# Kernel tuning notes

Hardware: AMD Instinct MI355X
Metric: run time of the kernel (lower is better)

## Reference

```python
import jax, jax.numpy as jnp
import numpy as np

BN_EPS = 1e-5

def _bn(h, g, b):
    # BatchNorm1d training-mode math: biased batch stats over the node axis.
    m = h.mean(axis=0)
    v = h.var(axis=0)
    return (h - m) * jax.lax.rsqrt(v + BN_EPS) * g + b

def setup_inputs() -> dict:
    key = jax.random.key(0)
    ks = jax.random.split(key, 8)
    N, E, D_IN, H, L = 50000, 800000, 128, 256, 3
    return {
        "x": jax.random.normal(ks[0], (N, D_IN), dtype=jnp.float32),
        "edge_index": jax.random.randint(ks[1], (2, E), 0, N, dtype=jnp.int64),
        "eps": jnp.zeros((L,), dtype=jnp.float32),
        "W1_0": jax.random.normal(ks[2], (D_IN, H), dtype=jnp.float32),
        "W1_rest": jax.random.normal(ks[3], (L - 1, H, H), dtype=jnp.float32),
        "b1": jnp.zeros((L, H), dtype=jnp.float32),
        "g1": jnp.ones((L, H), dtype=jnp.float32),
        "bt1": jnp.zeros((L, H), dtype=jnp.float32),
        "W2": jax.random.normal(ks[4], (L, H, H), dtype=jnp.float32),
        "b2": jnp.zeros((L, H), dtype=jnp.float32),
        "g2": jnp.ones((L, H), dtype=jnp.float32),
        "bt2": jnp.zeros((L, H), dtype=jnp.float32),
    }

def reference(x, edge_index, eps, W1_0, W1_rest, b1, g1, bt1, W2, b2, g2, bt2):
    N = x.shape[0]
    row, col = edge_index[0], edge_index[1]
    L = eps.shape[0]

    def gin_layer(h, eps_i, Wa, ba, ga, bta, Wb, bb, gb, btb):
        # sum_{u in N(v)} h_u : gather source feats, scatter-add to dest rows
        agg = jax.ops.segment_sum(h[col], row, num_segments=N)
        out = (1.0 + eps_i) * h + agg
        out = _bn(out @ Wa + ba, ga, bta)        # Linear -> BN
        out = jax.nn.relu(out)                    # ReLU
        out = _bn(out @ Wb + bb, gb, btb)        # Linear -> BN
        return out

    h = x
    for i in range(L):
        Wa = W1_0 if i == 0 else W1_rest[i - 1]
        h = gin_layer(h, eps[i], Wa, b1[i], g1[i], bt1[i], W2[i], b2[i], g2[i], bt2[i])
        if i < L - 1:
            h = jax.nn.relu(h)  # inter-layer ReLU; dropout is identity in eval mode
    return h
```

## Files before the change

### kernel.cpp

```cpp
#include <hip/hip_runtime.h>
#include <hip/hip_bf16.h>
#include <math.h>
#include <stdint.h>

typedef short short8 __attribute__((ext_vector_type(8)));
typedef float f32x4 __attribute__((ext_vector_type(4)));

__device__ __forceinline__ float bf2f(unsigned int u) {
    union { unsigned int i; float f; } x; x.i = u << 16; return x.f;
}
__device__ __forceinline__ unsigned short f2bf(float f) {
    union { float f; unsigned int i; } x; x.f = f;
    unsigned int r = x.i + 0x7fffu + ((x.i >> 16) & 1u);
    return (unsigned short)(r >> 16);
}

__global__ void hist_k(const int* __restrict__ row, int* __restrict__ deg, int E) {
    int e = blockIdx.x * blockDim.x + threadIdx.x;
    if (e < E) atomicAdd(&deg[row[e]], 1);
}
__global__ void block_sums(const int* __restrict__ deg, int* __restrict__ bs, int N) {
    __shared__ int tmp[256];
    int t = threadIdx.x;
    int i = blockIdx.x * 256 + t;
    tmp[t] = (i < N) ? deg[i] : 0;
    __syncthreads();
    for (int off = 128; off > 0; off >>= 1) {
        if (t < off) tmp[t] += tmp[t + off];
        __syncthreads();
    }
    if (t == 0) bs[blockIdx.x] = tmp[0];
}
__global__ void scan_bs(const int* __restrict__ bs, int* __restrict__ bo, int B) {
    __shared__ int tmp[256];
    int t = threadIdx.x;
    int v = (t < B) ? bs[t] : 0;
    tmp[t] = v;
    __syncthreads();
    for (int off = 1; off < 256; off <<= 1) {
        int x = (t >= off) ? tmp[t - off] : 0;
        __syncthreads();
        tmp[t] += x;
        __syncthreads();
    }
    bo[t] = tmp[t] - v;
}
__global__ void finalize_rowptr(const int* __restrict__ deg, const int* __restrict__ bo,
                                int* __restrict__ rowptr, int* __restrict__ cursor,
                                int N, int E) {
    __shared__ int tmp[256];
    int t = threadIdx.x;
    int i = blockIdx.x * 256 + t;
    int v = (i < N) ? deg[i] : 0;
    tmp[t] = v;
    __syncthreads();
    for (int off = 1; off < 256; off <<= 1) {
        int x = (t >= off) ? tmp[t - off] : 0;
        __syncthreads();
        tmp[t] += x;
        __syncthreads();
    }
    int excl = tmp[t] - v + bo[blockIdx.x];
    if (i < N) { rowptr[i] = excl; cursor[i] = excl; }
    if (i == N) rowptr[N] = E;
}
__global__ void fill_csr(const int* __restrict__ row, const int* __restrict__ col,
                         int* __restrict__ cursor, int* __restrict__ idx, int E) {
    int e = blockIdx.x * blockDim.x + threadIdx.x;
    if (e < E) {
        int p = atomicAdd(&cursor[row[e]], 1);
        idx[p] = col[e];
    }
}

__global__ void zero_all(int* __restrict__ deg, int n_deg,
                         uint4* __restrict__ a, uint4* __restrict__ b, uint4* __restrict__ c,
                         int n_t, uint4* __restrict__ st, int n_st) {
    int i = blockIdx.x * blockDim.x + threadIdx.x;
    uint4 z = make_uint4(0, 0, 0, 0);
    if (i < n_deg) deg[i] = 0;
    if (i < n_t) { a[i] = z; b[i] = z; c[i] = z; }
    if (i < n_st) st[i] = z;
}

__global__ void prep_all(const float* __restrict__ x, unsigned short* __restrict__ xb, int nconv,
                         const float* __restrict__ W1_0, const float* __restrict__ W1rest,
                         const float* __restrict__ W2, unsigned short* __restrict__ wt) {
    int i = blockIdx.x * blockDim.x + threadIdx.x;
    if (i < nconv) {
        float4 v = *(const float4*)(x + (size_t)i * 4);
        unsigned int lo = (unsigned int)f2bf(v.x) | ((unsigned int)f2bf(v.y) << 16);
        unsigned int hi = (unsigned int)f2bf(v.z) | ((unsigned int)f2bf(v.w) << 16);
        *(uint2*)(xb + (size_t)i * 4) = make_uint2(lo, hi);
        return;
    }
    int id = i - nconv;
    if (id < 32768) {
        int k = id >> 8, c = id & 255;
        wt[c * 128 + k] = f2bf(W1_0[id]);
    } else if (id < 163840) {
        int t = id - 32768;
        int m = t >> 16, r = t & 65535;
        int k = r >> 8, c = r & 255;
        wt[32768 + m * 65536 + c * 256 + k] = f2bf(W1rest[t]);
    } else if (id < 360448) {
        int t = id - 163840;
        int m = t >> 16, r = t & 65535;
        int k = r >> 8, c = r & 255;
        wt[163840 + m * 65536 + c * 256 + k] = f2bf(W2[t]);
    }
}

template<int H, bool FUSE_BN>
__global__ __launch_bounds__(256) void aggregate_f(
    const unsigned short* __restrict__ h,
    const int* __restrict__ rowptr, const int* __restrict__ idx,
    const float* __restrict__ eps_p, int layer,
    const float* __restrict__ stats, const float* __restrict__ g,
    const float* __restrict__ bt, float invN,
    unsigned short* __restrict__ out, int N) {
    constexpr int NW = H / 128;
    int lane = threadIdx.x & 63;
    int v = blockIdx.x * 4 + (threadIdx.x >> 6);
    if (v >= N) return;

    float sc[2 * NW], sh[2 * NW];
    if constexpr (FUSE_BN) {
#pragma unroll
        for (int j = 0; j < 2 * NW; ++j) {
            int c = lane * 2 * NW + j;
            float m = stats[c] * invN;
            float var = stats[256 + c] * invN - m * m;
            sc[j] = g[c] * rsqrtf(var + 1e-5f);
            sh[j] = bt[c] - m * sc[j];
        }
    }
    const float s = 1.f + eps_p[layer];
    const unsigned int* hu = (const unsigned int*)h;

    float acc[2 * NW];
    {
        const unsigned int* hv = hu + (size_t)v * (H / 2) + lane * NW;
#pragma unroll
        for (int j = 0; j < NW; ++j) {
            unsigned int r = hv[j];
            float f0 = bf2f(r & 0xffffu), f1 = bf2f(r >> 16);
            if constexpr (FUSE_BN) {
                f0 = fmaxf(f0 * sc[2 * j] + sh[2 * j], 0.f);
                f1 = fmaxf(f1 * sc[2 * j + 1] + sh[2 * j + 1], 0.f);
            }
            acc[2 * j] = s * f0;
            acc[2 * j + 1] = s * f1;
        }
    }
    int e = rowptr[v], end = rowptr[v + 1];
    for (; e + 3 < end; e += 4) {
        int u0 = idx[e], u1 = idx[e + 1], u2 = idx[e + 2], u3 = idx[e + 3];
        const unsigned int* q0 = hu + (size_t)u0 * (H / 2) + lane * NW;
        const unsigned int* q1 = hu + (size_t)u1 * (H / 2) + lane * NW;
        const unsigned int* q2 = hu + (size_t)u2 * (H / 2) + lane * NW;
        const unsigned int* q3 = hu + (size_t)u3 * (H / 2) + lane * NW;
        unsigned int r0[NW], r1[NW], r2[NW], r3[NW];
#pragma unroll
        for (int j = 0; j < NW; ++j) { r0[j] = q0[j]; r1[j] = q1[j]; r2[j] = q2[j]; r3[j] = q3[j]; }
#pragma unroll
        for (int j = 0; j < NW; ++j) {
            float a0 = bf2f(r0[j] & 0xffffu), b0 = bf2f(r0[j] >> 16);
            float a1 = bf2f(r1[j] & 0xffffu), b1 = bf2f(r1[j] >> 16);
            float a2 = bf2f(r2[j] & 0xffffu), b2 = bf2f(r2[j] >> 16);
            float a3 = bf2f(r3[j] & 0xffffu), b3 = bf2f(r3[j] >> 16);
            if constexpr (FUSE_BN) {
                float c0 = sc[2 * j], d0 = sh[2 * j], c1 = sc[2 * j + 1], d1 = sh[2 * j + 1];
                a0 = fmaxf(a0 * c0 + d0, 0.f); b0 = fmaxf(b0 * c1 + d1, 0.f);
                a1 = fmaxf(a1 * c0 + d0, 0.f); b1 = fmaxf(b1 * c1 + d1, 0.f);
                a2 = fmaxf(a2 * c0 + d0, 0.f); b2 = fmaxf(b2 * c1 + d1, 0.f);
                a3 = fmaxf(a3 * c0 + d0, 0.f); b3 = fmaxf(b3 * c1 + d1, 0.f);
            }
            acc[2 * j]     += (a0 + a1) + (a2 + a3);
            acc[2 * j + 1] += (b0 + b1) + (b2 + b3);
        }
    }
    for (; e < end; ++e) {
        const unsigned int* q = hu + (size_t)idx[e] * (H / 2) + lane * NW;
#pragma unroll
        for (int j = 0; j < NW; ++j) {
            unsigned int r = q[j];
            float f0 = bf2f(r & 0xffffu), f1 = bf2f(r >> 16);
            if constexpr (FUSE_BN) {
                f0 = fmaxf(f0 * sc[2 * j] + sh[2 * j], 0.f);
                f1 = fmaxf(f1 * sc[2 * j + 1] + sh[2 * j + 1], 0.f);
            }
            acc[2 * j] += f0;
            acc[2 * j + 1] += f1;
        }
    }
    unsigned int* op = (unsigned int*)out + (size_t)v * (H / 2) + lane * NW;
#pragma unroll
    for (int j = 0; j < NW; ++j)
        op[j] = (unsigned int)f2bf(acc[2 * j]) | ((unsigned int)f2bf(acc[2 * j + 1]) << 16);
}

template<int K, bool TRANS_A>
__global__ __launch_bounds__(256) void gemm_mfma(const unsigned short* __restrict__ A,
                                                 const unsigned short* __restrict__ Wt,
                                                 const float* __restrict__ bias,
                                                 const float* __restrict__ stats_in,
                                                 const float* __restrict__ gp,
                                                 const float* __restrict__ btp,
                                                 float invN,
                                                 unsigned short* __restrict__ Y,
                                                 float* __restrict__ stats_out,
                                                 int Nrows) {
    __shared__ unsigned short sA[2][128 * 32];
    __shared__ unsigned short sB[2][128 * 32];
    __shared__ float reds[128], redq[128];
    __shared__ float spc[256], sps[256];
    const int tid = threadIdx.x;
    const int lane = tid & 63;
    const int wid = tid >> 6;
    const int wm = wid >> 1, wn = wid & 1;
    const int r0 = blockIdx.x * 128;
    const int c0 = blockIdx.y * 128;
    const int chunk0 = wid * 2;
    const int akk = (lane & 3) * 8;
    const int arow_l = lane >> 2;

    if constexpr (TRANS_A) {
        float m = stats_in[tid] * invN;
        float var = stats_in[256 + tid] * invN - m * m;
        float sv = gp[tid] * rsqrtf(var + 1e-5f);
        spc[tid] = sv;
        sps[tid] = btp[tid] - m * sv;
        __syncthreads();
    }

    f32x4 acc[4][4] = {};

    auto stageB = [&](int buf, int k0) {
#pragma unroll
        for (int q = 0; q < 2; ++q) {
            int chunk = chunk0 + q;
            int byteoff = chunk * 1024 + lane * 16;
            int row = byteoff >> 6;
            int kk = (byteoff & 63) >> 1;
            const unsigned short* gB = Wt + (size_t)(c0 + row) * K + k0 + kk;
            __builtin_amdgcn_global_load_lds(
                (const __attribute__((address_space(1))) void*)(uintptr_t)gB,
                (__attribute__((address_space(3))) void*)(uintptr_t)(&sB[buf][chunk * 512]),
                16, 0, 0);
        }
    };
    auto stageA_direct = [&](int buf, int k0) {
#pragma unroll
        for (int q = 0; q < 2; ++q) {
            int chunk = chunk0 + q;
            int byteoff = chunk * 1024 + lane * 16;
            int row = byteoff >> 6;
            int kk = (byteoff & 63) >> 1;
            const unsigned short* gA = A + (size_t)(r0 + row) * K + k0 + kk;
            __builtin_amdgcn_global_load_lds(
                (const __attribute__((address_space(1))) void*)(uintptr_t)gA,
                (__attribute__((address_space(3))) void*)(uintptr_t)(&sA[buf][chunk * 512]),
                16, 0, 0);
        }
    };
    uint4 areg[2];
    auto loadA = [&](int k0) {
#pragma unroll
        for (int q = 0; q < 2; ++q) {
            int row = (chunk0 + q) * 16 + arow_l;
            areg[q] = *(const uint4*)(A + (size_t)(r0 + row) * K + k0 + akk);
        }
    };
    auto writeA = [&](int buf, int k0) {
        float4 sca = *(const float4*)&spc[k0 + akk];
        float4 scb = *(const float4*)&spc[k0 + akk + 4];
        float4 sha = *(const float4*)&sps[k0 + akk];
        float4 shb = *(const float4*)&sps[k0 + akk + 4];
#pragma unroll
        for (int q = 0; q < 2; ++q) {
            uint4 u = areg[q];
            float f0 = fmaxf(bf2f(u.x & 0xffffu) * sca.x + sha.x, 0.f);
            float f1 = fmaxf(bf2f(u.x >> 16)     * sca.y + sha.y, 0.f);
            float f2 = fmaxf(bf2f(u.y & 0xffffu) * sca.z + sha.z, 0.f);
            float f3 = fmaxf(bf2f(u.y >> 16)     * sca.w + sha.w, 0.f);
            float f4 = fmaxf(bf2f(u.z & 0xffffu) * scb.x + shb.x, 0.f);
            float f5 = fmaxf(bf2f(u.z >> 16)     * scb.y + shb.y, 0.f);
            float f6 = fmaxf(bf2f(u.w & 0xffffu) * scb.z + shb.z, 0.f);
            float f7 = fmaxf(bf2f(u.w >> 16)     * scb.w + shb.w, 0.f);
            uint4 w;
            w.x = (unsigned int)f2bf(f0) | ((unsigned int)f2bf(f1) << 16);
            w.y = (unsigned int)f2bf(f2) | ((unsigned int)f2bf(f3) << 16);
            w.z = (unsigned int)f2bf(f4) | ((unsigned int)f2bf(f5) << 16);
            w.w = (unsigned int)f2bf(f6) | ((unsigned int)f2bf(f7) << 16);
            *(uint4*)&sA[buf][(chunk0 + q) * 512 + lane * 8] = w;
        }
    };

    const int nt = K / 32;
    if constexpr (TRANS_A) { loadA(0); } else { stageA_direct(0, 0); }
    stageB(0, 0);
    const int krow = lane >> 4;
    const int rl = lane & 15;

    for (int t = 0; t < nt; ++t) {
        if constexpr (TRANS_A) writeA(t & 1, t * 32);
        __syncthreads();
        if (t + 1 < nt) {
            stageB((t + 1) & 1, (t + 1) * 32);
            if constexpr (TRANS_A) loadA((t + 1) * 32);
            else stageA_direct((t + 1) & 1, (t + 1) * 32);
        }
        const unsigned short* sAb = sA[t & 1];
        const unsigned short* sBb = sB[t & 1];
        short8 a[4], b[4];
#pragma unroll
        for (int i = 0; i < 4; ++i) {
            a[i] = *(const short8*)(sAb + (wm * 64 + i * 16 + rl) * 32 + krow * 8);
            b[i] = *(const short8*)(sBb + (wn * 64 + i * 16 + rl) * 32 + krow * 8);
        }
#pragma unroll
        for (int i = 0; i < 4; ++i)
#pragma unroll
            for (int n = 0; n < 4; ++n)
                asm volatile("v_mfma_f32_16x16x32_bf16 %0, %1, %2, %0"
                             : "+v"(acc[i][n])
                             : "v"(a[i]), "v"(b[n]));
    }
    asm volatile("s_nop 7\n\ts_nop 7" ::);

    const int rg = lane >> 4;
    float ssum[4], qsum[4];
#pragma unroll
    for (int n = 0; n < 4; ++n) {
        int col = c0 + wn * 64 + n * 16 + rl;
        float bvv = bias[col];
        float s = 0.f, q2 = 0.f;
#pragma unroll
        for (int i = 0; i < 4; ++i) {
#pragma unroll
            for (int r = 0; r < 4; ++r) {
                int grow = r0 + wm * 64 + i * 16 + rg * 4 + r;
                if (grow < Nrows) {
                    float v = acc[i][n][r] + bvv;
                    Y[(size_t)grow * 256 + col] = f2bf(v);
                    s += v;
                    q2 += v * v;
                }
            }
        }
        s  += __shfl_xor(s, 16, 64);  s  += __shfl_xor(s, 32, 64);
        q2 += __shfl_xor(q2, 16, 64); q2 += __shfl_xor(q2, 32, 64);
        ssum[n] = s; qsum[n] = q2;
    }
    if (wm == 0 && rg == 0) {
#pragma unroll
        for (int n = 0; n < 4; ++n) {
            int lc = wn * 64 + n * 16 + rl;
            reds[lc] = ssum[n];
            redq[lc] = qsum[n];
        }
    }
    __syncthreads();
    if (wm == 1 && rg == 0) {
#pragma unroll
        for (int n = 0; n < 4; ++n) {
            int lc = wn * 64 + n * 16 + rl;
            int c = c0 + lc;
            atomicAdd(&stats_out[c], ssum[n] + reds[lc]);
            atomicAdd(&stats_out[256 + c], qsum[n] + redq[lc]);
        }
    }
}

__global__ void bn_fuse(const unsigned short* __restrict__ Y, const float* __restrict__ stats,
                        const float* __restrict__ g, const float* __restrict__ bt,
                        float invN, float* __restrict__ outf, int total8) {
    int i = blockIdx.x * blockDim.x + threadIdx.x;
    if (i >= total8) return;
    int col0 = (i & 31) << 3;
    uint4 y = ((const uint4*)Y)[i];
    unsigned int yy[4] = {y.x, y.y, y.z, y.w};
    float o[8];
#pragma unroll
    for (int j = 0; j < 4; ++j) {
        o[2 * j]     = bf2f(yy[j] & 0xffffu);
        o[2 * j + 1] = bf2f(yy[j] >> 16);
    }
#pragma unroll
    for (int j = 0; j < 8; ++j) {
        int c = col0 + j;
        float mean = stats[c] * invN;
        float var = stats[256 + c] * invN - mean * mean;
        float sc = g[c] * rsqrtf(var + 1e-5f);
        float sh = bt[c] - mean * sc;
        o[j] = o[j] * sc + sh;
    }
    float4* of = (float4*)outf;
    of[2 * i]     = make_float4(o[0], o[1], o[2], o[3]);
    of[2 * i + 1] = make_float4(o[4], o[5], o[6], o[7]);
}

extern "C" void kernel_launch(void* const* d_in, const int* in_sizes, int n_in,
                              void* d_out, int out_size, void* d_ws, size_t ws_size,
                              hipStream_t stream) {
    const float* x      = (const float*)d_in[0];
    const int*   ei     = (const int*)d_in[1];
    const float* eps    = (const float*)d_in[2];
    const float* W1_0   = (const float*)d_in[3];
    const float* W1rest = (const float*)d_in[4];
    const float* b1     = (const float*)d_in[5];
    const float* g1     = (const float*)d_in[6];
    const float* bt1    = (const float*)d_in[7];
    const float* W2     = (const float*)d_in[8];
    const float* b2     = (const float*)d_in[9];
    const float* g2     = (const float*)d_in[10];
    const float* bt2    = (const float*)d_in[11];

    const int N = in_sizes[0] / 128;
    const int E = in_sizes[1] / 2;
    const int* row = ei;
    const int* col = ei + E;
    const int Npad = ((N + 127) / 128) * 128;
    const int nbRow = Npad / 128;

    char* w = (char*)d_ws;
    auto alloc = [&](size_t bytes) {
        char* p = w;
        w += (bytes + 255) & ~(size_t)255;
        return p;
    };
    unsigned short* xb = (unsigned short*)alloc((size_t)Npad * 128 * 2);
    unsigned short* p0 = (unsigned short*)alloc((size_t)Npad * 256 * 2);
    unsigned short* p1 = (unsigned short*)alloc((size_t)Npad * 256 * 2);
    unsigned short* Yb = (unsigned short*)alloc((size_t)Npad * 256 * 2);
    unsigned short* wt = (unsigned short*)alloc((size_t)360448 * 2);
    float* stats  = (float*)alloc(3072 * 4);
    int* deg    = (int*)alloc((size_t)N * 4);
    int* cursor = (int*)alloc((size_t)N * 4);
    int* rowptr = (int*)alloc((size_t)(N + 1) * 4);
    int* bs     = (int*)alloc(256 * 4);
    int* bo     = (int*)alloc(256 * 4);
    int* idxb   = (int*)alloc((size_t)E * 4);

    const float invN = 1.f / (float)N;
    const int B = (N + 255) / 256;

    int tail16 = (Npad - N) * 256 * 2 / 16;
    {
        uint4* t0 = (uint4*)(p0 + (size_t)N * 256);
        uint4* t1 = (uint4*)(p1 + (size_t)N * 256);
        uint4* t2 = (uint4*)(Yb + (size_t)N * 256);
        int mx = N;
        if (tail16 > mx) mx = tail16;
        if (768 > mx) mx = 768;
        zero_all<<<(mx + 255) / 256, 256, 0, stream>>>(deg, N, t0, t1, t2, tail16,
                                                       (uint4*)stats, 768);
    }

    hist_k<<<(E + 255) / 256, 256, 0, stream>>>(row, deg, E);
    block_sums<<<B, 256, 0, stream>>>(deg, bs, N);
    scan_bs<<<1, 256, 0, stream>>>(bs, bo, B);
    finalize_rowptr<<<B, 256, 0, stream>>>(deg, bo, rowptr, cursor, N, E);
    fill_csr<<<(E + 255) / 256, 256, 0, stream>>>(row, col, cursor, idxb, E);

    const int nconv = N * 32;
    prep_all<<<(nconv + 360448 + 255) / 256, 256, 0, stream>>>(x, xb, nconv,
                                                               W1_0, W1rest, W2, wt);

    const int aggGrid = (N + 3) / 4;
    const int bnGrid = (N * 32 + 255) / 256;
    dim3 gg(nbRow, 2);

    for (int layer = 0; layer < 3; ++layer) {
        float* st1 = stats + layer * 1024;
        float* st2 = st1 + 512;
        float* st2p = stats + (layer - 1) * 1024 + 512;

        if (layer == 0)
            aggregate_f<128, false><<<aggGrid, 256, 0, stream>>>(
                xb, rowptr, idxb, eps, 0, nullptr, nullptr, nullptr, invN, p1, N);
        else
            aggregate_f<256, true><<<aggGrid, 256, 0, stream>>>(
                p0, rowptr, idxb, eps, layer, st2p,
                g2 + (layer - 1) * 256, bt2 + (layer - 1) * 256, invN, p1, N);

        if (layer == 0)
            gemm_mfma<128, false><<<gg, 256, 0, stream>>>(
                p1, wt, b1, nullptr, nullptr, nullptr, invN, Yb, st1, N);
        else
            gemm_mfma<256, false><<<gg, 256, 0, stream>>>(
                p1, wt + 32768 + (size_t)(layer - 1) * 65536, b1 + layer * 256,
                nullptr, nullptr, nullptr, invN, Yb, st1, N);

        gemm_mfma<256, true><<<gg, 256, 0, stream>>>(
            Yb, wt + 163840 + (size_t)layer * 65536, b2 + layer * 256,
            st1, g1 + layer * 256, bt1 + layer * 256, invN, p0, st2, N);
    }

    bn_fuse<<<bnGrid, 256, 0, stream>>>(p0, stats + 2 * 1024 + 512,
                                        g2 + 2 * 256, bt2 + 2 * 256,
                                        invN, (float*)d_out, N * 32);
}
```

Baseline: 491.1 us.

## Widen GEMM tile to full 256 columns with 512-thread blocks, fold histogram into prep

Each GEMM block now computes a 128x256 output tile with 8 waves instead of two 128x128 blocks per row strip. The A tile, including the BN+ReLU transform in the second GEMM, is loaded and converted once instead of twice, which removes redundant A traffic and duplicate normalization work. The degree histogram is merged into the prep kernel to save one launch. The trade-off is more LDS per block, fewer blocks (one per 128 rows), and possibly lower occupancy.

```diff
diff --git a/kernel.cpp b/kernel.cpp
--- a/kernel.cpp
+++ b/kernel.cpp
@@ -15,10 +15,6 @@
     return (unsigned short)(r >> 16);
 }
 
-__global__ void hist_k(const int* __restrict__ row, int* __restrict__ deg, int E) {
-    int e = blockIdx.x * blockDim.x + threadIdx.x;
-    if (e < E) atomicAdd(&deg[row[e]], 1);
-}
 __global__ void block_sums(const int* __restrict__ deg, int* __restrict__ bs, int N) {
     __shared__ int tmp[256];
     int t = threadIdx.x;
@@ -85,7 +81,8 @@
 
 __global__ void prep_all(const float* __restrict__ x, unsigned short* __restrict__ xb, int nconv,
                          const float* __restrict__ W1_0, const float* __restrict__ W1rest,
-                         const float* __restrict__ W2, unsigned short* __restrict__ wt) {
+                         const float* __restrict__ W2, unsigned short* __restrict__ wt,
+                         const int* __restrict__ erow, int* __restrict__ deg, int E) {
     int i = blockIdx.x * blockDim.x + threadIdx.x;
     if (i < nconv) {
         float4 v = *(const float4*)(x + (size_t)i * 4);
@@ -98,17 +95,22 @@
     if (id < 32768) {
         int k = id >> 8, c = id & 255;
         wt[c * 128 + k] = f2bf(W1_0[id]);
+        return;
     } else if (id < 163840) {
         int t = id - 32768;
         int m = t >> 16, r = t & 65535;
         int k = r >> 8, c = r & 255;
         wt[32768 + m * 65536 + c * 256 + k] = f2bf(W1rest[t]);
+        return;
     } else if (id < 360448) {
         int t = id - 163840;
         int m = t >> 16, r = t & 65535;
         int k = r >> 8, c = r & 255;
         wt[163840 + m * 65536 + c * 256 + k] = f2bf(W2[t]);
-    }
+        return;
+    }
+    int e = id - 360448;
+    if (e < E) atomicAdd(&deg[erow[e]], 1);
 }
 
 template<int H, bool FUSE_BN>
@@ -201,7 +203,7 @@
 }
 
 template<int K, bool TRANS_A>
-__global__ __launch_bounds__(256) void gemm_mfma(const unsigned short* __restrict__ A,
+__global__ __launch_bounds__(512) void gemm_mfma(const unsigned short* __restrict__ A,
                                                  const unsigned short* __restrict__ Wt,
                                                  const float* __restrict__ bias,
                                                  const float* __restrict__ stats_in,
@@ -212,25 +214,26 @@
                                                  float* __restrict__ stats_out,
                                                  int Nrows) {
     __shared__ unsigned short sA[2][128 * 32];
-    __shared__ unsigned short sB[2][128 * 32];
-    __shared__ float reds[128], redq[128];
+    __shared__ unsigned short sB[2][256 * 32];
+    __shared__ float reds[256], redq[256];
     __shared__ float spc[256], sps[256];
     const int tid = threadIdx.x;
     const int lane = tid & 63;
     const int wid = tid >> 6;
-    const int wm = wid >> 1, wn = wid & 1;
+    const int wm = wid >> 2;
+    const int wn = wid & 3;
     const int r0 = blockIdx.x * 128;
-    const int c0 = blockIdx.y * 128;
-    const int chunk0 = wid * 2;
-    const int akk = (lane & 3) * 8;
-    const int arow_l = lane >> 2;
+    const int arow = tid >> 2;
+    const int akk = (tid & 3) * 8;
 
     if constexpr (TRANS_A) {
-        float m = stats_in[tid] * invN;
-        float var = stats_in[256 + tid] * invN - m * m;
-        float sv = gp[tid] * rsqrtf(var + 1e-5f);
-        spc[tid] = sv;
-        sps[tid] = btp[tid] - m * sv;
+        if (tid < 256) {
+            float m = stats_in[tid] * invN;
+            float var = stats_in[256 + tid] * invN - m * m;
+            float sv = gp[tid] * rsqrtf(var + 1e-5f);
+            spc[tid] = sv;
+            sps[tid] = btp[tid] - m * sv;
+        }
         __syncthreads();
     }
 
@@ -239,62 +242,45 @@
     auto stageB = [&](int buf, int k0) {
 #pragma unroll
         for (int q = 0; q < 2; ++q) {
-            int chunk = chunk0 + q;
-            int byteoff = chunk * 1024 + lane * 16;
-            int row = byteoff >> 6;
-            int kk = (byteoff & 63) >> 1;
-            const unsigned short* gB = Wt + (size_t)(c0 + row) * K + k0 + kk;
+            int row = q * 128 + arow;
+            const unsigned short* gB = Wt + (size_t)row * K + k0 + akk;
             __builtin_amdgcn_global_load_lds(
                 (const __attribute__((address_space(1))) void*)(uintptr_t)gB,
-                (__attribute__((address_space(3))) void*)(uintptr_t)(&sB[buf][chunk * 512]),
+                (__attribute__((address_space(3))) void*)(uintptr_t)(&sB[buf][q * 4096 + tid * 8]),
                 16, 0, 0);
         }
     };
     auto stageA_direct = [&](int buf, int k0) {
-#pragma unroll
-        for (int q = 0; q < 2; ++q) {
-            int chunk = chunk0 + q;
-            int byteoff = chunk * 1024 + lane * 16;
-            int row = byteoff >> 6;
-            int kk = (byteoff & 63) >> 1;
-            const unsigned short* gA = A + (size_t)(r0 + row) * K + k0 + kk;
-            __builtin_amdgcn_global_load_lds(
-                (const __attribute__((address_space(1))) void*)(uintptr_t)gA,
-                (__attribute__((address_space(3))) void*)(uintptr_t)(&sA[buf][chunk * 512]),
-                16, 0, 0);
-        }
+        const unsigned short* gA = A + (size_t)(r0 + arow) * K + k0 + akk;
+        __builtin_amdgcn_global_load_lds(
+            (const __attribute__((address_space(1))) void*)(uintptr_t)gA,
+            (__attribute__((address_space(3))) void*)(uintptr_t)(&sA[buf][tid * 8]),
+            16, 0, 0);
     };
-    uint4 areg[2];
+    uint4 areg;
     auto loadA = [&](int k0) {
-#pragma unroll
-        for (int q = 0; q < 2; ++q) {
-            int row = (chunk0 + q) * 16 + arow_l;
-            areg[q] = *(const uint4*)(A + (size_t)(r0 + row) * K + k0 + akk);
-        }
+        areg = *(const uint4*)(A + (size_t)(r0 + arow) * K + k0 + akk);
     };
     auto writeA = [&](int buf, int k0) {
         float4 sca = *(const float4*)&spc[k0 + akk];
         float4 scb = *(const float4*)&spc[k0 + akk + 4];
         float4 sha = *(const float4*)&sps[k0 + akk];
         float4 shb = *(const float4*)&sps[k0 + akk + 4];
-#pragma unroll
-        for (int q = 0; q < 2; ++q) {
-            uint4 u = areg[q];
-            float f0 = fmaxf(bf2f(u.x & 0xffffu) * sca.x + sha.x, 0.f);
-            float f1 = fmaxf(bf2f(u.x >> 16)     * sca.y + sha.y, 0.f);
-            float f2 = fmaxf(bf2f(u.y & 0xffffu) * sca.z + sha.z, 0.f);
-            float f3 = fmaxf(bf2f(u.y >> 16)     * sca.w + sha.w, 0.f);
-            float f4 = fmaxf(bf2f(u.z & 0xffffu) * scb.x + shb.x, 0.f);
-            float f5 = fmaxf(bf2f(u.z >> 16)     * scb.y + shb.y, 0.f);
-            float f6 = fmaxf(bf2f(u.w & 0xffffu) * scb.z + shb.z, 0.f);
-            float f7 = fmaxf(bf2f(u.w >> 16)     * scb.w + shb.w, 0.f);
-            uint4 w;
-            w.x = (unsigned int)f2bf(f0) | ((unsigned int)f2bf(f1) << 16);
-            w.y = (unsigned int)f2bf(f2) | ((unsigned int)f2bf(f3) << 16);
-            w.z = (unsigned int)f2bf(f4) | ((unsigned int)f2bf(f5) << 16);
-            w.w = (unsigned int)f2bf(f6) | ((unsigned int)f2bf(f7) << 16);
-            *(uint4*)&sA[buf][(chunk0 + q) * 512 + lane * 8] = w;
-        }
+        uint4 u = areg;
+        float f0 = fmaxf(bf2f(u.x & 0xffffu) * sca.x + sha.x, 0.f);
+        float f1 = fmaxf(bf2f(u.x >> 16)     * sca.y + sha.y, 0.f);
+        float f2 = fmaxf(bf2f(u.y & 0xffffu) * sca.z + sha.z, 0.f);
+        float f3 = fmaxf(bf2f(u.y >> 16)     * sca.w + sha.w, 0.f);
+        float f4 = fmaxf(bf2f(u.z & 0xffffu) * scb.x + shb.x, 0.f);
+        float f5 = fmaxf(bf2f(u.z >> 16)     * scb.y + shb.y, 0.f);
+        float f6 = fmaxf(bf2f(u.w & 0xffffu) * scb.z + shb.z, 0.f);
+        float f7 = fmaxf(bf2f(u.w >> 16)     * scb.w + shb.w, 0.f);
+        uint4 w;
+        w.x = (unsigned int)f2bf(f0) | ((unsigned int)f2bf(f1) << 16);
+        w.y = (unsigned int)f2bf(f2) | ((unsigned int)f2bf(f3) << 16);
+        w.z = (unsigned int)f2bf(f4) | ((unsigned int)f2bf(f5) << 16);
+        w.w = (unsigned int)f2bf(f6) | ((unsigned int)f2bf(f7) << 16);
+        *(uint4*)&sA[buf][tid * 8] = w;
     };
 
     const int nt = K / 32;
@@ -333,7 +319,7 @@
     float ssum[4], qsum[4];
 #pragma unroll
     for (int n = 0; n < 4; ++n) {
-        int col = c0 + wn * 64 + n * 16 + rl;
+        int col = wn * 64 + n * 16 + rl;
         float bvv = bias[col];
         float s = 0.f, q2 = 0.f;
 #pragma unroll
@@ -366,9 +352,8 @@
 #pragma unroll
         for (int n = 0; n < 4; ++n) {
             int lc = wn * 64 + n * 16 + rl;
-            int c = c0 + lc;
-            atomicAdd(&stats_out[c], ssum[n] + reds[lc]);
-            atomicAdd(&stats_out[256 + c], qsum[n] + redq[lc]);
+            atomicAdd(&stats_out[lc], ssum[n] + reds[lc]);
+            atomicAdd(&stats_out[256 + lc], qsum[n] + redq[lc]);
         }
     }
 }
@@ -458,19 +443,21 @@
                                                        (uint4*)stats, 768);
     }
 
-    hist_k<<<(E + 255) / 256, 256, 0, stream>>>(row, deg, E);
+    const int nconv = N * 32;
+    {
+        int total = nconv + 360448 + E;
+        prep_all<<<(total + 255) / 256, 256, 0, stream>>>(x, xb, nconv,
+                                                          W1_0, W1rest, W2, wt,
+                                                          row, deg, E);
+    }
+
     block_sums<<<B, 256, 0, stream>>>(deg, bs, N);
     scan_bs<<<1, 256, 0, stream>>>(bs, bo, B);
     finalize_rowptr<<<B, 256, 0, stream>>>(deg, bo, rowptr, cursor, N, E);
     fill_csr<<<(E + 255) / 256, 256, 0, stream>>>(row, col, cursor, idxb, E);
 
-    const int nconv = N * 32;
-    prep_all<<<(nconv + 360448 + 255) / 256, 256, 0, stream>>>(x, xb, nconv,
-                                                               W1_0, W1rest, W2, wt);
-
     const int aggGrid = (N + 3) / 4;
     const int bnGrid = (N * 32 + 255) / 256;
-    dim3 gg(nbRow, 2);
 
     for (int layer = 0; layer < 3; ++layer) {
         float* st1 = stats + layer * 1024;
@@ -486,14 +473,14 @@
                 g2 + (layer - 1) * 256, bt2 + (layer - 1) * 256, invN, p1, N);
 
         if (layer == 0)
-            gemm_mfma<128, false><<<gg, 256, 0, stream>>>(
+            gemm_mfma<128, false><<<nbRow, 512, 0, stream>>>(
                 p1, wt, b1, nullptr, nullptr, nullptr, invN, Yb, st1, N);
         else
-            gemm_mfma<256, false><<<gg, 256, 0, stream>>>(
+            gemm_mfma<256, false><<<nbRow, 512, 0, stream>>>(
                 p1, wt + 32768 + (size_t)(layer - 1) * 65536, b1 + layer * 256,
                 nullptr, nullptr, nullptr, invN, Yb, st1, N);
 
-        gemm_mfma<256, true><<<gg, 256, 0, stream>>>(
+        gemm_mfma<256, true><<<nbRow, 512, 0, stream>>>(
             Yb, wt + 163840 + (size_t)layer * 65536, b2 + layer * 256,
             st1, g1 + layer * 256, bt1 + layer * 256, invN, p0, st2, N);
     }
```

Measured after the change: 436.2 us (median of 2 runs). -11.2%, faster.
